# Kernel optimization log

Measured on AMD Instinct MI355X. Metric: run time of the kernel, lower is better.

Reference implementation:

```python
import jax, jax.numpy as jnp
import numpy as np

N_NODES = 1_000_000
N_EDGES = 16_000_000


def setup_inputs() -> dict:
    key = jax.random.key(0)
    k1, k2, k3, k4 = jax.random.split(key, 4)
    x = jax.random.normal(k1, (N_NODES, 2), dtype=jnp.float32)
    edge_index = jax.random.randint(k2, (2, N_EDGES), 0, N_NODES, dtype=jnp.int64)
    W1 = jax.random.normal(k3, (2, 4), dtype=jnp.float32) * 0.5
    b1 = jnp.zeros((4,), dtype=jnp.float32)
    W2 = jax.random.normal(k4, (4, 2), dtype=jnp.float32) * 0.5
    b2 = jnp.zeros((2,), dtype=jnp.float32)
    return {"x": x, "edge_index": edge_index, "W1": W1, "b1": b1, "W2": W2, "b2": b2}


def _gcn_conv(h, src, dst, norm, b, n_nodes):
    # h already linearly transformed: message = h[src] * norm, scatter-add to dst
    msg = h[src] * norm[:, None]
    out = jax.ops.segment_sum(msg, dst, num_segments=n_nodes)
    return out + b


def reference(x, edge_index, W1, b1, W2, b2):
    n = x.shape[0]
    loop = jnp.arange(n, dtype=edge_index.dtype)
    # PyG GCNConv default: add self-loops, symmetric deg^{-1/2} normalization
    src = jnp.concatenate([edge_index[0], loop])
    dst = jnp.concatenate([edge_index[1], loop])
    deg = jax.ops.segment_sum(jnp.ones_like(src, dtype=x.dtype), dst, num_segments=n)
    dinv = jnp.where(deg > 0, jax.lax.rsqrt(deg), 0.0)
    norm = dinv[src] * dinv[dst]

    h = _gcn_conv(x @ W1, src, dst, norm, b1, n)   # conv1: [N,2] -> [N,4]
    h = jax.nn.relu(h)
    out = _gcn_conv(h @ W2, src, dst, norm, b2, n)  # conv2: [N,4] -> [N,2]
    return out
```

## Files before the change

kernel.cpp:

```cpp
#include <hip/hip_runtime.h>
#include <hip/hip_fp16.h>


constexpr int W_SHIFT = 11;
constexpr int W = 2048;
constexpr int MAXB = 512;
constexpr int RB = 1024;
constexpr int CHUNK = 8192;
constexpr int AB = 512;

constexpr float SCALE1 = 65536.0f;
constexpr float INV1   = 1.0f / 65536.0f;
constexpr unsigned BIAS1 = 1u << 20;
constexpr float SCALE2 = 4096.0f;
constexpr float INV2   = 1.0f / 4096.0f;
constexpr unsigned BIAS2 = 1u << 22;

typedef unsigned uv4 __attribute__((ext_vector_type(4)));
typedef int      iv4 __attribute__((ext_vector_type(4)));

__device__ __forceinline__ unsigned long long pack2(float a, float b,
                                                    float scale, unsigned bias) {
    unsigned lo = (unsigned)(__float2int_rn(a * scale) + (int)bias);
    unsigned hi = (unsigned)(__float2int_rn(b * scale) + (int)bias);
    return (unsigned long long)lo | ((unsigned long long)hi << 32);
}

__global__ __launch_bounds__(256) void k_zero_fill(unsigned* __restrict__ fill,
                                                   int nb, unsigned C) {
    int i = blockIdx.x * 256 + threadIdx.x;
    if (i < nb) fill[i] = (unsigned)i * C;
}

__global__ __launch_bounds__(RB) void k_reorder(const int* __restrict__ src,
                                                const int* __restrict__ dst,
                                                unsigned* __restrict__ fill,
                                                unsigned* __restrict__ perm, int E) {
    __shared__ unsigned hist[MAXB];
    __shared__ unsigned lbase[MAXB];
    __shared__ unsigned gdelta[MAXB];
    __shared__ unsigned sorted[CHUNK];
    __shared__ unsigned short sbb[CHUNK];
    int tid = threadIdx.x;
    if (tid < MAXB) hist[tid] = 0u;
    __syncthreads();
    long base0 = (long)blockIdx.x * CHUNK;
    int total = (int)min((long)CHUNK, (long)E - base0);
    bool full = (total == CHUNK);

    if (full) {
        const iv4* dv4 = (const iv4*)(dst + base0);
        #pragma unroll
        for (int k = 0; k < 2; k++) {
            iv4 q = dv4[k * RB + tid];
            atomicAdd(&hist[((unsigned)q.x) >> W_SHIFT], 1u);
            atomicAdd(&hist[((unsigned)q.y) >> W_SHIFT], 1u);
            atomicAdd(&hist[((unsigned)q.z) >> W_SHIFT], 1u);
            atomicAdd(&hist[((unsigned)q.w) >> W_SHIFT], 1u);
        }
    } else {
        for (int li = tid; li < total; li += RB)
            atomicAdd(&hist[((unsigned)dst[base0 + li]) >> W_SHIFT], 1u);
    }
    __syncthreads();
    unsigned v = (tid < MAXB) ? hist[tid] : 0u;
    if (tid < MAXB) lbase[tid] = v;
    __syncthreads();
    for (int off = 1; off < MAXB; off <<= 1) {
        unsigned u = (tid >= off && tid < MAXB) ? lbase[tid - off] : 0u;
        __syncthreads();
        if (tid < MAXB) lbase[tid] += u;
        __syncthreads();
    }
    if (tid < MAXB) {
        unsigned excl = lbase[tid] - v;
        unsigned gd = 0u;
        if (v) gd = atomicAdd(&fill[tid], v) - excl;
        gdelta[tid] = gd;
        hist[tid] = excl;
    }
    __syncthreads();
    if (full) {
        const iv4* dv4 = (const iv4*)(dst + base0);
        const iv4* sv4 = (const iv4*)(src + base0);
        #pragma unroll
        for (int k = 0; k < 2; k++) {
            iv4 dq = dv4[k * RB + tid];
            iv4 sq = sv4[k * RB + tid];
            unsigned d, b, lpos;
            d = (unsigned)dq.x; b = d >> W_SHIFT; lpos = atomicAdd(&hist[b], 1u);
            sorted[lpos] = (unsigned)sq.x | ((d & (W - 1)) << 20); sbb[lpos] = (unsigned short)b;
            d = (unsigned)dq.y; b = d >> W_SHIFT; lpos = atomicAdd(&hist[b], 1u);
            sorted[lpos] = (unsigned)sq.y | ((d & (W - 1)) << 20); sbb[lpos] = (unsigned short)b;
            d = (unsigned)dq.z; b = d >> W_SHIFT; lpos = atomicAdd(&hist[b], 1u);
            sorted[lpos] = (unsigned)sq.z | ((d & (W - 1)) << 20); sbb[lpos] = (unsigned short)b;
            d = (unsigned)dq.w; b = d >> W_SHIFT; lpos = atomicAdd(&hist[b], 1u);
            sorted[lpos] = (unsigned)sq.w | ((d & (W - 1)) << 20); sbb[lpos] = (unsigned short)b;
        }
    } else {
        for (int li = tid; li < total; li += RB) {
            unsigned d = (unsigned)dst[base0 + li];
            unsigned s = (unsigned)src[base0 + li];
            unsigned b = d >> W_SHIFT;
            unsigned lpos = atomicAdd(&hist[b], 1u);
            sorted[lpos] = s | ((d & (W - 1)) << 20);
            sbb[lpos] = (unsigned short)b;
        }
    }
    __syncthreads();
    if (full) {
        #pragma unroll
        for (int k = 0; k < CHUNK / RB; k++) {
            int t = k * RB + tid;
            unsigned b = sbb[t];
            perm[gdelta[b] + t] = sorted[t];
        }
    } else {
        for (int t = tid; t < total; t += RB) {
            unsigned b = sbb[t];
            perm[gdelta[b] + t] = sorted[t];
        }
    }
}

__global__ __launch_bounds__(AB) void k_dinv(const unsigned* __restrict__ perm,
                                             const unsigned* __restrict__ fill,
                                             const float2* __restrict__ x,
                                             float* __restrict__ dinv,
                                             unsigned* __restrict__ deg,
                                             __half2* __restrict__ xs,
                                             int N, unsigned C) {
    __shared__ unsigned c[2 * W];
    for (int i = threadIdx.x; i < 2 * W; i += AB) c[i] = 0u;
    __syncthreads();
    int b = blockIdx.x;
    unsigned par = threadIdx.x & 1u;
    unsigned s = (unsigned)b * C, e = fill[b];
    unsigned m = e - s, nv8 = m >> 3;
    const uv4* p4 = (const uv4*)(perm + s);
    for (unsigned j = threadIdx.x; j < nv8; j += AB) {
        uv4 qa = __builtin_nontemporal_load(p4 + 2u * j);
        uv4 qb = __builtin_nontemporal_load(p4 + 2u * j + 1u);
        atomicAdd(&c[((qa.x >> 20) << 1) | par], 1u);
        atomicAdd(&c[((qa.y >> 20) << 1) | par], 1u);
        atomicAdd(&c[((qa.z >> 20) << 1) | par], 1u);
        atomicAdd(&c[((qa.w >> 20) << 1) | par], 1u);
        atomicAdd(&c[((qb.x >> 20) << 1) | par], 1u);
        atomicAdd(&c[((qb.y >> 20) << 1) | par], 1u);
        atomicAdd(&c[((qb.z >> 20) << 1) | par], 1u);
        atomicAdd(&c[((qb.w >> 20) << 1) | par], 1u);
    }
    unsigned t = s + (nv8 << 3) + threadIdx.x;
    if (t < e) atomicAdd(&c[((perm[t] >> 20) << 1) | par], 1u);
    __syncthreads();
    int d0 = b << W_SHIFT;
    for (int l = threadIdx.x; l < W; l += AB) {
        int d = d0 + l;
        if (d < N) {
            unsigned cn = c[2 * l] + c[2 * l + 1];
            float dv = 1.0f / sqrtf((float)(cn + 1u));
            dinv[d] = dv;
            deg[d] = cn;
            float2 xv = x[d];
            xs[d] = __floats2half2_rn(xv.x * dv, xv.y * dv);
        }
    }
}

__global__ __launch_bounds__(AB) void k_acc1(const unsigned* __restrict__ perm,
                                             const unsigned* __restrict__ fill,
                                             const __half2* __restrict__ xs,
                                             const float* __restrict__ dinv,
                                             const unsigned* __restrict__ deg,
                                             const float* __restrict__ W1,
                                             const float* __restrict__ b1,
                                             const float* __restrict__ W2,
                                             __half2* __restrict__ h2s,
                                             int N, unsigned C) {
    __shared__ unsigned long long acc[2 * W];
    for (int i = threadIdx.x; i < 2 * W; i += AB) acc[i] = 0ull;
    __syncthreads();
    int b = blockIdx.x;
    unsigned par = threadIdx.x & 1u;
    unsigned s = (unsigned)b * C, e = fill[b];
    unsigned m = e - s, nv8 = m >> 3;
    const uv4* p4 = (const uv4*)(perm + s);
    for (unsigned j = threadIdx.x; j < nv8; j += AB) {
        uv4 qa = __builtin_nontemporal_load(p4 + 2u * j);
        uv4 qb = __builtin_nontemporal_load(p4 + 2u * j + 1u);
        float2 v0 = __half22float2(xs[qa.x & 0xFFFFFu]);
        float2 v1 = __half22float2(xs[qa.y & 0xFFFFFu]);
        float2 v2 = __half22float2(xs[qa.z & 0xFFFFFu]);
        float2 v3 = __half22float2(xs[qa.w & 0xFFFFFu]);
        float2 v4 = __half22float2(xs[qb.x & 0xFFFFFu]);
        float2 v5 = __half22float2(xs[qb.y & 0xFFFFFu]);
        float2 v6 = __half22float2(xs[qb.z & 0xFFFFFu]);
        float2 v7 = __half22float2(xs[qb.w & 0xFFFFFu]);
        atomicAdd(&acc[((qa.x >> 20) << 1) | par], pack2(v0.x, v0.y, SCALE1, BIAS1));
        atomicAdd(&acc[((qa.y >> 20) << 1) | par], pack2(v1.x, v1.y, SCALE1, BIAS1));
        atomicAdd(&acc[((qa.z >> 20) << 1) | par], pack2(v2.x, v2.y, SCALE1, BIAS1));
        atomicAdd(&acc[((qa.w >> 20) << 1) | par], pack2(v3.x, v3.y, SCALE1, BIAS1));
        atomicAdd(&acc[((qb.x >> 20) << 1) | par], pack2(v4.x, v4.y, SCALE1, BIAS1));
        atomicAdd(&acc[((qb.y >> 20) << 1) | par], pack2(v5.x, v5.y, SCALE1, BIAS1));
        atomicAdd(&acc[((qb.z >> 20) << 1) | par], pack2(v6.x, v6.y, SCALE1, BIAS1));
        atomicAdd(&acc[((qb.w >> 20) << 1) | par], pack2(v7.x, v7.y, SCALE1, BIAS1));
    }
    unsigned t = s + (nv8 << 3) + threadIdx.x;
    if (t < e) {
        unsigned p = perm[t];
        float2 v = __half22float2(xs[p & 0xFFFFFu]);
        atomicAdd(&acc[((p >> 20) << 1) | par], pack2(v.x, v.y, SCALE1, BIAS1));
    }
    __syncthreads();
    int d0 = b << W_SHIFT;
    float w10 = W1[0], w11 = W1[1], w12 = W1[2], w13 = W1[3];
    float w14 = W1[4], w15 = W1[5], w16 = W1[6], w17 = W1[7];
    float bb0 = b1[0], bb1 = b1[1], bb2 = b1[2], bb3 = b1[3];
    float u0 = W2[0], u1 = W2[1], u2 = W2[2], u3 = W2[3];
    float u4 = W2[4], u5 = W2[5], u6 = W2[6], u7 = W2[7];
    for (int l = threadIdx.x; l < W; l += AB) {
        int d = d0 + l;
        if (d < N) {
            float dv = dinv[d];
            unsigned cn = deg[d];
            unsigned long long a64 = acc[2 * l] + acc[2 * l + 1];
            unsigned lo = (unsigned)a64, hi = (unsigned)(a64 >> 32);
            float2 self = __half22float2(xs[d]);
            float Sx = (float)(int)(lo - cn * BIAS1) * INV1 + self.x;
            float Sy = (float)(int)(hi - cn * BIAS1) * INV1 + self.y;
            float a0 = fmaxf(fmaf(Sy, w14, Sx * w10) * dv + bb0, 0.0f);
            float a1 = fmaxf(fmaf(Sy, w15, Sx * w11) * dv + bb1, 0.0f);
            float a2 = fmaxf(fmaf(Sy, w16, Sx * w12) * dv + bb2, 0.0f);
            float a3 = fmaxf(fmaf(Sy, w17, Sx * w13) * dv + bb3, 0.0f);
            float hx = (a0 * u0 + a1 * u2 + a2 * u4 + a3 * u6) * dv;
            float hy = (a0 * u1 + a1 * u3 + a2 * u5 + a3 * u7) * dv;
            h2s[d] = __floats2half2_rn(hx, hy);
        }
    }
}

__global__ __launch_bounds__(AB) void k_acc2(const unsigned* __restrict__ perm,
                                             const unsigned* __restrict__ fill,
                                             const __half2* __restrict__ h2s,
                                             const float* __restrict__ dinv,
                                             const unsigned* __restrict__ deg,
                                             const float* __restrict__ b2,
                                             float2* __restrict__ out,
                                             int N, unsigned C) {
    __shared__ unsigned long long acc[2 * W];
    for (int i = threadIdx.x; i < 2 * W; i += AB) acc[i] = 0ull;
    __syncthreads();
    int b = blockIdx.x;
    unsigned par = threadIdx.x & 1u;
    unsigned s = (unsigned)b * C, e = fill[b];
    unsigned m = e - s, nv8 = m >> 3;
    const uv4* p4 = (const uv4*)(perm + s);
    for (unsigned j = threadIdx.x; j < nv8; j += AB) {
        uv4 qa = __builtin_nontemporal_load(p4 + 2u * j);
        uv4 qb = __builtin_nontemporal_load(p4 + 2u * j + 1u);
        float2 v0 = __half22float2(h2s[qa.x & 0xFFFFFu]);
        float2 v1 = __half22float2(h2s[qa.y & 0xFFFFFu]);
        float2 v2 = __half22float2(h2s[qa.z & 0xFFFFFu]);
        float2 v3 = __half22float2(h2s[qa.w & 0xFFFFFu]);
        float2 v4 = __half22float2(h2s[qb.x & 0xFFFFFu]);
        float2 v5 = __half22float2(h2s[qb.y & 0xFFFFFu]);
        float2 v6 = __half22float2(h2s[qb.z & 0xFFFFFu]);
        float2 v7 = __half22float2(h2s[qb.w & 0xFFFFFu]);
        atomicAdd(&acc[((qa.x >> 20) << 1) | par], pack2(v0.x, v0.y, SCALE2, BIAS2));
        atomicAdd(&acc[((qa.y >> 20) << 1) | par], pack2(v1.x, v1.y, SCALE2, BIAS2));
        atomicAdd(&acc[((qa.z >> 20) << 1) | par], pack2(v2.x, v2.y, SCALE2, BIAS2));
        atomicAdd(&acc[((qa.w >> 20) << 1) | par], pack2(v3.x, v3.y, SCALE2, BIAS2));
        atomicAdd(&acc[((qb.x >> 20) << 1) | par], pack2(v4.x, v4.y, SCALE2, BIAS2));
        atomicAdd(&acc[((qb.y >> 20) << 1) | par], pack2(v5.x, v5.y, SCALE2, BIAS2));
        atomicAdd(&acc[((qb.z >> 20) << 1) | par], pack2(v6.x, v6.y, SCALE2, BIAS2));
        atomicAdd(&acc[((qb.w >> 20) << 1) | par], pack2(v7.x, v7.y, SCALE2, BIAS2));
    }
    unsigned t = s + (nv8 << 3) + threadIdx.x;
    if (t < e) {
        unsigned p = perm[t];
        float2 v = __half22float2(h2s[p & 0xFFFFFu]);
        atomicAdd(&acc[((p >> 20) << 1) | par], pack2(v.x, v.y, SCALE2, BIAS2));
    }
    __syncthreads();
    int d0 = b << W_SHIFT;
    float bb0 = b2[0], bb1 = b2[1];
    for (int l = threadIdx.x; l < W; l += AB) {
        int d = d0 + l;
        if (d < N) {
            float dv = dinv[d];
            unsigned cn = deg[d];
            unsigned long long a64 = acc[2 * l] + acc[2 * l + 1];
            unsigned lo = (unsigned)a64, hi = (unsigned)(a64 >> 32);
            float2 v = __half22float2(h2s[d]);
            float Sx = (float)(int)(lo - cn * BIAS2) * INV2 + v.x;
            float Sy = (float)(int)(hi - cn * BIAS2) * INV2 + v.y;
            out[d] = make_float2(Sx * dv + bb0, Sy * dv + bb1);
        }
    }
}


__global__ __launch_bounds__(256) void f_init_deg(unsigned* deg, int n) {
    int i = blockIdx.x * 256 + threadIdx.x;
    if (i < n) deg[i] = 1u;
}
__global__ __launch_bounds__(256) void f_count_deg(const int* dst, unsigned* deg, int E) {
    int e = blockIdx.x * 256 + threadIdx.x;
    if (e < E) atomicAdd(&deg[dst[e]], 1u);
}
__global__ __launch_bounds__(256) void f_node1(const float2* x, const float* W1,
                                               const unsigned* deg, float* dinv,
                                               float4* h1s, float4* agg1, int n) {
    int i = blockIdx.x * 256 + threadIdx.x;
    if (i >= n) return;
    float dv = 1.0f / sqrtf((float)deg[i]);
    dinv[i] = dv;
    float2 xv = x[i];
    float4 h;
    h.x = fmaf(xv.y, W1[4], xv.x * W1[0]) * dv;
    h.y = fmaf(xv.y, W1[5], xv.x * W1[1]) * dv;
    h.z = fmaf(xv.y, W1[6], xv.x * W1[2]) * dv;
    h.w = fmaf(xv.y, W1[7], xv.x * W1[3]) * dv;
    h1s[i] = h;
    agg1[i] = make_float4(h.x * dv, h.y * dv, h.z * dv, h.w * dv);
}
__global__ __launch_bounds__(256) void f_edge1(const int* src, const int* dst,
                                               const float* dinv, const float4* h1s,
                                               float* agg1, int E) {
    int e = blockIdx.x * 256 + threadIdx.x;
    if (e >= E) return;
    int s = src[e], d = dst[e];
    float w = dinv[d];
    float4 m = h1s[s];
    float* p = agg1 + 4ll * d;
    unsafeAtomicAdd(p + 0, m.x * w);
    unsafeAtomicAdd(p + 1, m.y * w);
    unsafeAtomicAdd(p + 2, m.z * w);
    unsafeAtomicAdd(p + 3, m.w * w);
}
__global__ __launch_bounds__(256) void f_node2(const float4* agg1, const float* b1,
                                               const float* W2, const float* b2,
                                               const float* dinv, float2* h2s,
                                               float2* out, int n) {
    int i = blockIdx.x * 256 + threadIdx.x;
    if (i >= n) return;
    float4 a = agg1[i];
    a.x = fmaxf(a.x + b1[0], 0.0f);
    a.y = fmaxf(a.y + b1[1], 0.0f);
    a.z = fmaxf(a.z + b1[2], 0.0f);
    a.w = fmaxf(a.w + b1[3], 0.0f);
    float dv = dinv[i];
    float2 h;
    h.x = (a.x * W2[0] + a.y * W2[2] + a.z * W2[4] + a.w * W2[6]) * dv;
    h.y = (a.x * W2[1] + a.y * W2[3] + a.z * W2[5] + a.w * W2[7]) * dv;
    h2s[i] = h;
    out[i] = make_float2(b2[0] + h.x * dv, b2[1] + h.y * dv);
}
__global__ __launch_bounds__(256) void f_edge2(const int* src, const int* dst,
                                               const float* dinv, const float2* h2s,
                                               float* out, int E) {
    int e = blockIdx.x * 256 + threadIdx.x;
    if (e >= E) return;
    int s = src[e], d = dst[e];
    float w = dinv[d];
    float2 m = h2s[s];
    float* p = out + 2ll * d;
    unsafeAtomicAdd(p + 0, m.x * w);
    unsafeAtomicAdd(p + 1, m.y * w);
}

extern "C" void kernel_launch(void* const* d_in, const int* in_sizes, int n_in,
                              void* d_out, int out_size, void* d_ws, size_t ws_size,
                              hipStream_t stream) {
    const float* x  = (const float*)d_in[0];
    const int* ei   = (const int*)d_in[1];
    const float* W1 = (const float*)d_in[2];
    const float* b1 = (const float*)d_in[3];
    const float* W2 = (const float*)d_in[4];
    const float* b2 = (const float*)d_in[5];
    float* out = (float*)d_out;

    const int N = in_sizes[0] / 2;
    const int E = in_sizes[1] / 2;
    const int* src = ei;
    const int* dst = ei + E;
    const int NB = (N + W - 1) >> W_SHIFT;

    char* ws = (char*)d_ws;
    const int gN = (N + 255) / 256;
    const int gE = (E + 255) / 256;

    size_t fixed = 32768 + (size_t)16 * N;
    long avail = (long)ws_size - (long)fixed;
    long Cmax = (avail > 0) ? avail / (4L * NB) : 0;
    long Cmin = (long)(E / (NB > 0 ? NB : 1)) + 4096;
    long Cw = (Cmax > Cmin + 8192) ? (Cmin + 8192) : Cmax;
    unsigned C = (unsigned)(Cw & ~7L);
    bool fast = ((long)C >= Cmin) && (NB <= MAXB) && (N <= (1 << 20));

    if (fast) {
        unsigned* fill = (unsigned*)(ws);
        float*    dinv = (float*)(ws + 32768);
        unsigned* deg  = (unsigned*)(ws + 32768 + (size_t)4 * N);
        __half2*  xs   = (__half2*)(ws + 32768 + (size_t)8 * N);
        __half2*  h2s  = (__half2*)(ws + 32768 + (size_t)12 * N);
        unsigned* perm = (unsigned*)(ws + fixed);

        k_zero_fill<<<(NB + 255) / 256, 256, 0, stream>>>(fill, NB, C);
        k_reorder<<<(E + CHUNK - 1) / CHUNK, RB, 0, stream>>>(src, dst, fill, perm, E);
        k_dinv<<<NB, AB, 0, stream>>>(perm, fill, (const float2*)x, dinv, deg, xs, N, C);
        k_acc1<<<NB, AB, 0, stream>>>(perm, fill, xs, dinv, deg, W1, b1, W2, h2s, N, C);
        k_acc2<<<NB, AB, 0, stream>>>(perm, fill, h2s, dinv, deg, b2, (float2*)out, N, C);
    } else {
        unsigned* deg = (unsigned*)(ws);
        float* dinv   = (float*)(ws + (size_t)4 * N);
        float* h1s    = (float*)(ws + (size_t)8 * N);
        float* agg1   = (float*)(ws + (size_t)24 * N);
        float* h2s    = h1s;

        f_init_deg<<<gN, 256, 0, stream>>>(deg, N);
        f_count_deg<<<gE, 256, 0, stream>>>(dst, deg, E);
        f_node1<<<gN, 256, 0, stream>>>((const float2*)x, W1, deg, dinv,
                                        (float4*)h1s, (float4*)agg1, N);
        f_edge1<<<gE, 256, 0, stream>>>(src, dst, dinv, (const float4*)h1s, agg1, E);
        f_node2<<<gN, 256, 0, stream>>>((const float4*)agg1, b1, W2, b2, dinv,
                                        (float2*)h2s, (float2*)out, N);
        f_edge2<<<gE, 256, 0, stream>>>(src, dst, dinv, (const float2*)h2s, out, E);
    }
}
```

Before: 432.9 us.

## Replace histogram+scan bucket sort with fixed-capacity shared slabs and global overflow

The reorder kernel no longer runs a histogram pass, prefix scan and local sort before scattering. Each block now appends edges straight into per-bucket shared-memory slabs of fixed capacity, and spills any overflow directly to global memory through atomics on the bucket fill counters. This drops one read pass of dst and several barrier-heavy scan steps. In exchange it adds global atomics for overflow entries, and the flush writes less contiguous data than the old sorted-chunk scatter.

```diff
diff --git a/kernel.cpp b/kernel.cpp
--- a/kernel.cpp
+++ b/kernel.cpp
@@ -7,6 +7,7 @@
 constexpr int MAXB = 512;
 constexpr int RB = 1024;
 constexpr int CHUNK = 8192;
+constexpr int CAP = 28;
 constexpr int AB = 512;
 
 constexpr float SCALE1 = 65536.0f;
@@ -36,50 +37,16 @@
                                                 const int* __restrict__ dst,
                                                 unsigned* __restrict__ fill,
                                                 unsigned* __restrict__ perm, int E) {
-    __shared__ unsigned hist[MAXB];
-    __shared__ unsigned lbase[MAXB];
-    __shared__ unsigned gdelta[MAXB];
-    __shared__ unsigned sorted[CHUNK];
-    __shared__ unsigned short sbb[CHUNK];
+    __shared__ unsigned slab[MAXB * CAP];
+    __shared__ unsigned ptr[MAXB];
+    __shared__ unsigned gbase[MAXB];
     int tid = threadIdx.x;
-    if (tid < MAXB) hist[tid] = 0u;
+    if (tid < MAXB) ptr[tid] = 0u;
     __syncthreads();
     long base0 = (long)blockIdx.x * CHUNK;
     int total = (int)min((long)CHUNK, (long)E - base0);
     bool full = (total == CHUNK);
 
-    if (full) {
-        const iv4* dv4 = (const iv4*)(dst + base0);
-        #pragma unroll
-        for (int k = 0; k < 2; k++) {
-            iv4 q = dv4[k * RB + tid];
-            atomicAdd(&hist[((unsigned)q.x) >> W_SHIFT], 1u);
-            atomicAdd(&hist[((unsigned)q.y) >> W_SHIFT], 1u);
-            atomicAdd(&hist[((unsigned)q.z) >> W_SHIFT], 1u);
-            atomicAdd(&hist[((unsigned)q.w) >> W_SHIFT], 1u);
-        }
-    } else {
-        for (int li = tid; li < total; li += RB)
-            atomicAdd(&hist[((unsigned)dst[base0 + li]) >> W_SHIFT], 1u);
-    }
-    __syncthreads();
-    unsigned v = (tid < MAXB) ? hist[tid] : 0u;
-    if (tid < MAXB) lbase[tid] = v;
-    __syncthreads();
-    for (int off = 1; off < MAXB; off <<= 1) {
-        unsigned u = (tid >= off && tid < MAXB) ? lbase[tid - off] : 0u;
-        __syncthreads();
-        if (tid < MAXB) lbase[tid] += u;
-        __syncthreads();
-    }
-    if (tid < MAXB) {
-        unsigned excl = lbase[tid] - v;
-        unsigned gd = 0u;
-        if (v) gd = atomicAdd(&fill[tid], v) - excl;
-        gdelta[tid] = gd;
-        hist[tid] = excl;
-    }
-    __syncthreads();
     if (full) {
         const iv4* dv4 = (const iv4*)(dst + base0);
         const iv4* sv4 = (const iv4*)(src + base0);
@@ -87,39 +54,50 @@
         for (int k = 0; k < 2; k++) {
             iv4 dq = dv4[k * RB + tid];
             iv4 sq = sv4[k * RB + tid];
-            unsigned d, b, lpos;
-            d = (unsigned)dq.x; b = d >> W_SHIFT; lpos = atomicAdd(&hist[b], 1u);
-            sorted[lpos] = (unsigned)sq.x | ((d & (W - 1)) << 20); sbb[lpos] = (unsigned short)b;
-            d = (unsigned)dq.y; b = d >> W_SHIFT; lpos = atomicAdd(&hist[b], 1u);
-            sorted[lpos] = (unsigned)sq.y | ((d & (W - 1)) << 20); sbb[lpos] = (unsigned short)b;
-            d = (unsigned)dq.z; b = d >> W_SHIFT; lpos = atomicAdd(&hist[b], 1u);
-            sorted[lpos] = (unsigned)sq.z | ((d & (W - 1)) << 20); sbb[lpos] = (unsigned short)b;
-            d = (unsigned)dq.w; b = d >> W_SHIFT; lpos = atomicAdd(&hist[b], 1u);
-            sorted[lpos] = (unsigned)sq.w | ((d & (W - 1)) << 20); sbb[lpos] = (unsigned short)b;
+            unsigned d, b, val, lpos;
+            d = (unsigned)dq.x; b = d >> W_SHIFT;
+            val = (unsigned)sq.x | ((d & (W - 1)) << 20);
+            lpos = atomicAdd(&ptr[b], 1u);
+            if (lpos < (unsigned)CAP) slab[b * CAP + lpos] = val;
+            else perm[atomicAdd(&fill[b], 1u)] = val;
+            d = (unsigned)dq.y; b = d >> W_SHIFT;
+            val = (unsigned)sq.y | ((d & (W - 1)) << 20);
+            lpos = atomicAdd(&ptr[b], 1u);
+            if (lpos < (unsigned)CAP) slab[b * CAP + lpos] = val;
+            else perm[atomicAdd(&fill[b], 1u)] = val;
+            d = (unsigned)dq.z; b = d >> W_SHIFT;
+            val = (unsigned)sq.z | ((d & (W - 1)) << 20);
+            lpos = atomicAdd(&ptr[b], 1u);
+            if (lpos < (unsigned)CAP) slab[b * CAP + lpos] = val;
+            else perm[atomicAdd(&fill[b], 1u)] = val;
+            d = (unsigned)dq.w; b = d >> W_SHIFT;
+            val = (unsigned)sq.w | ((d & (W - 1)) << 20);
+            lpos = atomicAdd(&ptr[b], 1u);
+            if (lpos < (unsigned)CAP) slab[b * CAP + lpos] = val;
+            else perm[atomicAdd(&fill[b], 1u)] = val;
         }
     } else {
         for (int li = tid; li < total; li += RB) {
             unsigned d = (unsigned)dst[base0 + li];
             unsigned s = (unsigned)src[base0 + li];
             unsigned b = d >> W_SHIFT;
-            unsigned lpos = atomicAdd(&hist[b], 1u);
-            sorted[lpos] = s | ((d & (W - 1)) << 20);
-            sbb[lpos] = (unsigned short)b;
+            unsigned val = s | ((d & (W - 1)) << 20);
+            unsigned lpos = atomicAdd(&ptr[b], 1u);
+            if (lpos < (unsigned)CAP) slab[b * CAP + lpos] = val;
+            else perm[atomicAdd(&fill[b], 1u)] = val;
         }
     }
     __syncthreads();
-    if (full) {
-        #pragma unroll
-        for (int k = 0; k < CHUNK / RB; k++) {
-            int t = k * RB + tid;
-            unsigned b = sbb[t];
-            perm[gdelta[b] + t] = sorted[t];
-        }
-    } else {
-        for (int t = tid; t < total; t += RB) {
-            unsigned b = sbb[t];
-            perm[gdelta[b] + t] = sorted[t];
-        }
+    if (tid < MAXB) {
+        unsigned cnt = min(ptr[tid], (unsigned)CAP);
+        gbase[tid] = cnt ? atomicAdd(&fill[tid], cnt) : 0u;
+        ptr[tid] = cnt;
+    }
+    __syncthreads();
+    for (int s = tid; s < MAXB * CAP; s += RB) {
+        int b = s / CAP;
+        int i = s - b * CAP;
+        if (i < (int)ptr[b]) perm[gbase[b] + i] = slab[s];
     }
 }
 
```

Result: no change. 431.3 us (-0.4%).
